# Kernel optimization log

Measured on AMD Instinct MI355X. Metric: run time of the kernel, lower is better.

The kernel has to match this reference:

```python
import jax, jax.numpy as jnp
import numpy as np

N = 50000          # nodes
E = 800000         # edges
H = 160            # hidden_dim = 32*5
HC = 32            # hidden_dim // 5 per-feature encoder width
LM = 768           # lm_input_dim
NUM_REL = 2
LEAK = 0.01        # nn.LeakyReLU default negative_slope


def leaky_relu(v):
    return jnp.where(v >= 0, v, LEAK * v)


def setup_inputs() -> dict:
    key = jax.random.key(0)
    ks = jax.random.split(key, 32)

    def lin(k, din, dout):
        kw, _ = jax.random.split(k)
        s = 1.0 / np.sqrt(din)
        W = jax.random.uniform(kw, (din, dout), jnp.float32, -s, s)
        b = jnp.zeros((dout,), jnp.float32)
        return W, b

    inp = {}
    inp["pre_x"] = jax.random.normal(ks[0], (N, LM), jnp.float32)
    inp["x"] = jnp.zeros((N, H), jnp.float32)  # dead input (overwritten in forward)
    inp["edge_index"] = jax.random.randint(ks[1], (2, E), 0, N, jnp.int32)
    inp["edge_type"] = jax.random.randint(ks[2], (E,), 0, NUM_REL, jnp.int32)
    inp["num_prop"] = jax.random.normal(ks[3], (N, 6), jnp.float32)
    inp["num_category"] = jax.random.normal(ks[4], (N, 11), jnp.float32)
    inp["des_tensor"] = jax.random.normal(ks[5], (N, LM), jnp.float32)
    inp["tweet_tensor"] = jax.random.normal(ks[6], (N, LM), jnp.float32)

    inp["W_np"], inp["b_np"] = lin(ks[7], 6, HC)
    inp["W_nc"], inp["b_nc"] = lin(ks[8], 11, HC)
    inp["W_des"], inp["b_des"] = lin(ks[9], LM, HC)
    inp["W_text"], inp["b_text"] = lin(ks[10], LM, HC)
    inp["W_tweet"], inp["b_tweet"] = lin(ks[11], LM, HC)
    inp["W_in"], inp["b_in"] = lin(ks[12], H, H)

    s = 1.0 / np.sqrt(H)
    inp["W_rel1"] = jax.random.uniform(ks[13], (NUM_REL, H, H), jnp.float32, -s, s)
    inp["W_root1"], inp["b_conv1"] = lin(ks[14], H, H)
    inp["W_rel2"] = jax.random.uniform(ks[15], (NUM_REL, H, H), jnp.float32, -s, s)
    inp["W_root2"], inp["b_conv2"] = lin(ks[16], H, H)

    inp["W_o1"], inp["b_o1"] = lin(ks[17], H, 80)
    inp["W_o2"], inp["b_o2"] = lin(ks[18], 80, 2)
    return inp


def rgcn_conv(h, src, dst, edge_type, W_rel, W_root, b):
    # PyG RGCNConv: per-relation mean aggregation + root transform + bias.
    out = h @ W_root + b
    for r in range(NUM_REL):
        w = (edge_type == r).astype(h.dtype)              # [E]
        msg = (h @ W_rel[r])[src] * w[:, None]            # [E, H] gather of transformed feats
        summed = jax.ops.segment_sum(msg, dst, num_segments=N)
        cnt = jax.ops.segment_sum(w, dst, num_segments=N)
        out = out + summed / jnp.maximum(cnt, 1.0)[:, None]
    return out


def reference(pre_x, x, edge_index, edge_type, num_prop, num_category, des_tensor,
              tweet_tensor, W_np, b_np, W_nc, b_nc, W_des, b_des, W_text, b_text,
              W_tweet, b_tweet, W_in, b_in, W_rel1, W_root1, b_conv1,
              W_rel2, W_root2, b_conv2, W_o1, b_o1, W_o2, b_o2):
    # Dropout is identity at inference.
    n = leaky_relu(num_prop @ W_np + b_np)
    c = leaky_relu(num_category @ W_nc + b_nc)
    d = leaky_relu(des_tensor @ W_des + b_des)
    tw = leaky_relu(tweet_tensor @ W_text + b_text)
    pre_t = leaky_relu(pre_x @ W_tweet + b_tweet)
    h = jnp.concatenate((n, c, d, tw, pre_t), axis=1)     # [N, 160]
    h = leaky_relu(h @ W_in + b_in)

    src, dst = edge_index[0], edge_index[1]
    h = rgcn_conv(h, src, dst, edge_type, W_rel1, W_root1, b_conv1)
    h = rgcn_conv(h, src, dst, edge_type, W_rel2, W_root2, b_conv2)

    em = leaky_relu(h @ W_o1 + b_o1)                      # [N, 80]
    out = em @ W_o2 + b_o2                                # [N, 2]
    return out, em
```

## Files before the change

### kernel.cpp

```cpp
#include <hip/hip_runtime.h>

#define NN 50000
#define EE 800000
#define HH 160
#define LMD 768
#define NBLK 196

typedef __attribute__((ext_vector_type(8))) short s8;
typedef __attribute__((ext_vector_type(4))) float f4;

__device__ __forceinline__ float lrelu(float v){ return v >= 0.f ? v : 0.01f*v; }

__device__ __forceinline__ short f2b(float f){
  unsigned int u = __float_as_uint(f);
  unsigned int r = (u + 0x7fffu + ((u >> 16) & 1u)) >> 16;
  return (short)r;
}
__device__ __forceinline__ float b2f(short s){
  return __uint_as_float(((unsigned int)(unsigned short)s) << 16);
}

struct WD { const float* s; short* d; int K; int C; };
struct WDs { WD w[11]; };
__global__ __launch_bounds__(256) void wt_k(WDs ds)
{
  WD w = ds.w[blockIdx.y];
  int idx = blockIdx.x*256 + threadIdx.x;
  if (idx < w.K * w.C) {
    int k = idx / w.C, c = idx - k*w.C;
    w.d[(size_t)c*w.K + k] = f2b(w.s[idx]);
  }
}

__global__ __launch_bounds__(256) void enc_small_k(
    const float* __restrict__ npx, const float* __restrict__ ncx,
    const float* __restrict__ Wnp, const float* __restrict__ bnp,
    const float* __restrict__ Wnc, const float* __restrict__ bnc,
    short* __restrict__ out)
{
  int gid = blockIdx.x*256 + threadIdx.x;
  int row = gid >> 6, c = gid & 63;
  if (row >= NN) return;
  float acc;
  if (c < 32) {
    acc = bnp[c];
    #pragma unroll
    for (int k = 0; k < 6; ++k) acc += npx[row*6+k]*Wnp[k*32+c];
  } else {
    int cc = c - 32;
    acc = bnc[cc];
    #pragma unroll
    for (int k = 0; k < 11; ++k) acc += ncx[row*11+k]*Wnc[k*32+cc];
  }
  out[(size_t)row*HH + c] = f2b(lrelu(acc));
}

template<int C, bool XBF, bool OUTF32>
__global__ __launch_bounds__(256) void mgemm_k(
    const void* __restrict__ Xv, int ldx,
    const short* __restrict__ WT, const float* __restrict__ bias,
    void* __restrict__ outv, int ldo, int K, int leaky)
{
  constexpr int NT = C/16;
  __shared__ __attribute__((aligned(16))) short Xs[128*40];
  __shared__ __attribute__((aligned(16))) short Ws[C*40];
  const int t = threadIdx.x;
  const int r0 = blockIdx.x*128;
  const int w = t >> 6, L = t & 63;
  const int lm = L & 15, lq = L >> 4;

  f4 acc[2][NT];
  #pragma unroll
  for (int i = 0; i < 2; ++i)
    #pragma unroll
    for (int j = 0; j < NT; ++j) acc[i][j] = (f4){0.f,0.f,0.f,0.f};

  for (int k0 = 0; k0 < K; k0 += 32) {
    #pragma unroll
    for (int i = t; i < 512; i += 256) {
      int row = i >> 2, kg = i & 3;
      int gr = r0 + row;
      s8 v;
      if (gr < NN) {
        if (XBF) {
          v = *(const s8*)((const short*)Xv + (size_t)gr*ldx + k0 + kg*8);
        } else {
          const float* xp = (const float*)Xv + (size_t)gr*ldx + k0 + kg*8;
          float4 a = *(const float4*)xp;
          float4 b = *(const float4*)(xp+4);
          v[0]=f2b(a.x); v[1]=f2b(a.y); v[2]=f2b(a.z); v[3]=f2b(a.w);
          v[4]=f2b(b.x); v[5]=f2b(b.y); v[6]=f2b(b.z); v[7]=f2b(b.w);
        }
      } else {
        v = (s8){0,0,0,0,0,0,0,0};
      }
      *(s8*)&Xs[row*40 + kg*8] = v;
    }
    for (int i = t; i < C*4; i += 256) {
      int c = i >> 2, kg = i & 3;
      *(s8*)&Ws[c*40 + kg*8] = *(const s8*)(WT + (size_t)c*K + k0 + kg*8);
    }
    __syncthreads();
    s8 a0 = *(const s8*)&Xs[(w*32 + lm)*40 + lq*8];
    s8 a1 = *(const s8*)&Xs[(w*32 + 16 + lm)*40 + lq*8];
    #pragma unroll
    for (int j = 0; j < NT; ++j) {
      s8 bf = *(const s8*)&Ws[(j*16 + lm)*40 + lq*8];
      acc[0][j] = __builtin_amdgcn_mfma_f32_16x16x32_bf16(a0, bf, acc[0][j], 0, 0, 0);
      acc[1][j] = __builtin_amdgcn_mfma_f32_16x16x32_bf16(a1, bf, acc[1][j], 0, 0, 0);
    }
    __syncthreads();
  }

  #pragma unroll
  for (int i = 0; i < 2; ++i) {
    #pragma unroll
    for (int j = 0; j < NT; ++j) {
      int col = j*16 + lm;
      float bv = bias ? bias[col] : 0.f;
      #pragma unroll
      for (int r = 0; r < 4; ++r) {
        int gr = r0 + w*32 + i*16 + lq*4 + r;
        if (gr < NN) {
          float v = acc[i][j][r] + bv;
          if (leaky) v = lrelu(v);
          if (OUTF32) ((float*)outv)[(size_t)gr*ldo + col] = v;
          else        ((short*)outv)[(size_t)gr*ldo + col] = f2b(v);
        }
      }
    }
  }
}

__global__ __launch_bounds__(256) void hist_k(
    const int* __restrict__ dst, const int* __restrict__ et, int* __restrict__ cnt2)
{
  int e = blockIdx.x*256 + threadIdx.x;
  if (e < EE) atomicAdd(&cnt2[et[e]*NN + dst[e]], 1);
}

__global__ __launch_bounds__(256) void inv_k(
    const int* __restrict__ cnt2, float* __restrict__ inv2, int* __restrict__ cntall)
{
  int i = blockIdx.x*256 + threadIdx.x;
  if (i >= NN) return;
  int c0 = cnt2[i], c1 = cnt2[NN + i];
  inv2[i]      = 1.f / (float)max(c0, 1);
  inv2[NN + i] = 1.f / (float)max(c1, 1);
  cntall[i] = c0 + c1;
}

__global__ __launch_bounds__(256) void scan1_k(
    const int* __restrict__ cntall, int* __restrict__ off1, int* __restrict__ partials)
{
  __shared__ int sh[256];
  int t = threadIdx.x;
  int i = blockIdx.x*256 + t;
  sh[t] = (i < NN) ? cntall[i] : 0;
  __syncthreads();
  for (int s = 1; s < 256; s <<= 1) {
    int add = (t >= s) ? sh[t-s] : 0;
    __syncthreads();
    sh[t] += add;
    __syncthreads();
  }
  if (i < NN) off1[i] = sh[t];
  if (t == 255) partials[blockIdx.x] = sh[255];
}

__global__ __launch_bounds__(256) void scan2_k(int* __restrict__ partials)
{
  __shared__ int sh[256];
  int t = threadIdx.x;
  sh[t] = (t < NBLK) ? partials[t] : 0;
  __syncthreads();
  for (int s = 1; s < 256; s <<= 1) {
    int add = (t >= s) ? sh[t-s] : 0;
    __syncthreads();
    sh[t] += add;
    __syncthreads();
  }
  if (t < NBLK) partials[t] = (t == 0) ? 0 : sh[t-1];
}

__global__ __launch_bounds__(256) void scan3_k(
    int* __restrict__ off, int* __restrict__ cursor, const int* __restrict__ partials)
{
  int i = blockIdx.x*256 + threadIdx.x;
  if (i < NN) {
    int v = off[i+1] + partials[i >> 8];
    off[i+1] = v;
    if (i + 1 < NN) cursor[i+1] = v;
  }
  if (i == 0) { off[0] = 0; cursor[0] = 0; }
}

__global__ __launch_bounds__(256) void scatter_k(
    const int* __restrict__ src, const int* __restrict__ dst, const int* __restrict__ et,
    int* __restrict__ cursor, int* __restrict__ elist)
{
  int e = blockIdx.x*256 + threadIdx.x;
  if (e >= EE) return;
  int d = dst[e];
  int pos = atomicAdd(&cursor[d], 1);
  elist[pos] = (src[e] << 1) | et[e];
}

__global__ __launch_bounds__(256) void aggregate_k(
    const int* __restrict__ off, const int* __restrict__ elist,
    const float* __restrict__ inv2,
    const short* __restrict__ t0, const short* __restrict__ t1,
    short* __restrict__ acc)
{
  int gid = blockIdx.x*256 + threadIdx.x;
  int d = gid / 20, q = gid - d*20;
  if (d >= NN) return;
  int beg = off[d], end = off[d+1];
  float i0 = inv2[d], i1 = inv2[NN + d];
  short* ap = acc + (size_t)d*HH + q*8;
  s8 rv = *(const s8*)ap;
  float a[8];
  #pragma unroll
  for (int i = 0; i < 8; ++i) a[i] = b2f(rv[i]);
  for (int p = beg; p < end; ++p) {
    int pk = elist[p];
    int s = pk >> 1;
    const short* tb = (pk & 1) ? t1 : t0;
    float sc = (pk & 1) ? i1 : i0;
    s8 v = *(const s8*)(tb + (size_t)s*HH + q*8);
    #pragma unroll
    for (int i = 0; i < 8; ++i) a[i] += b2f(v[i]) * sc;
  }
  s8 o;
  #pragma unroll
  for (int i = 0; i < 8; ++i) o[i] = f2b(a[i]);
  *(s8*)ap = o;
}

__global__ __launch_bounds__(256) void final_k(
    const float* __restrict__ em, const float* __restrict__ W,
    const float* __restrict__ b, float* __restrict__ out)
{
  int row = blockIdx.x*256 + threadIdx.x;
  if (row >= NN) return;
  float a0 = b[0], a1 = b[1];
  const float* e = em + (size_t)row*80;
  #pragma unroll
  for (int k = 0; k < 80; ++k) { float v = e[k]; a0 += v*W[k*2]; a1 += v*W[k*2+1]; }
  out[row*2] = a0; out[row*2+1] = a1;
}

extern "C" void kernel_launch(void* const* d_in, const int* in_sizes, int n_in,
                              void* d_out, int out_size, void* d_ws, size_t ws_size,
                              hipStream_t stream)
{
  const float* pre_x   = (const float*)d_in[0];
  const int*   eidx    = (const int*)d_in[2];
  const int*   etype   = (const int*)d_in[3];
  const float* num_prop= (const float*)d_in[4];
  const float* num_cat = (const float*)d_in[5];
  const float* des     = (const float*)d_in[6];
  const float* tweet   = (const float*)d_in[7];
  const float* W_np=(const float*)d_in[8],  *b_np=(const float*)d_in[9];
  const float* W_nc=(const float*)d_in[10], *b_nc=(const float*)d_in[11];
  const float* W_des=(const float*)d_in[12],*b_des=(const float*)d_in[13];
  const float* W_text=(const float*)d_in[14],*b_text=(const float*)d_in[15];
  const float* W_tweet=(const float*)d_in[16],*b_tweet=(const float*)d_in[17];
  const float* W_in=(const float*)d_in[18], *b_in=(const float*)d_in[19];
  const float* W_rel1=(const float*)d_in[20], *W_root1=(const float*)d_in[21], *b_c1=(const float*)d_in[22];
  const float* W_rel2=(const float*)d_in[23], *W_root2=(const float*)d_in[24], *b_c2=(const float*)d_in[25];
  const float* W_o1=(const float*)d_in[26], *b_o1=(const float*)d_in[27];
  const float* W_o2=(const float*)d_in[28], *b_o2=(const float*)d_in[29];

  float* out = (float*)d_out;
  float* em  = out + (size_t)NN*2;

  short* A  = (short*)d_ws;
  short* Bb = A  + (size_t)NN*HH;
  short* T0 = Bb + (size_t)NN*HH;
  short* T1 = T0 + (size_t)NN*HH;
  short* WT = T1 + (size_t)NN*HH;
  short* WT_des    = WT;
  short* WT_text   = WT +  24576;
  short* WT_tweet  = WT +  49152;
  short* WT_in     = WT +  73728;
  short* WT_root1  = WT +  99328;
  short* WT_rel1_0 = WT + 124928;
  short* WT_rel1_1 = WT + 150528;
  short* WT_root2  = WT + 176128;
  short* WT_rel2_0 = WT + 201728;
  short* WT_rel2_1 = WT + 227328;
  short* WT_o1     = WT + 252928;

  int*   cnt2    = (int*)(WT + 265728);
  float* inv2    = (float*)(cnt2 + 2*NN);
  int*   cntall  = (int*)(inv2 + 2*NN);
  int*   off     = cntall + NN;
  int*   partials= off + NN + 1;
  int*   cursor  = partials + 256;
  int*   elist   = cursor + NN;

  const int* src = eidx;
  const int* dst = eidx + EE;

  WDs ds;
  ds.w[0]  = (WD){W_des,          WT_des,    LMD, 32};
  ds.w[1]  = (WD){W_text,         WT_text,   LMD, 32};
  ds.w[2]  = (WD){W_tweet,        WT_tweet,  LMD, 32};
  ds.w[3]  = (WD){W_in,           WT_in,     HH, HH};
  ds.w[4]  = (WD){W_root1,        WT_root1,  HH, HH};
  ds.w[5]  = (WD){W_rel1,         WT_rel1_0, HH, HH};
  ds.w[6]  = (WD){W_rel1 + HH*HH, WT_rel1_1, HH, HH};
  ds.w[7]  = (WD){W_root2,        WT_root2,  HH, HH};
  ds.w[8]  = (WD){W_rel2,         WT_rel2_0, HH, HH};
  ds.w[9]  = (WD){W_rel2 + HH*HH, WT_rel2_1, HH, HH};
  ds.w[10] = (WD){W_o1,           WT_o1,     HH, 80};
  wt_k<<<dim3(100, 11), 256, 0, stream>>>(ds);

  hipMemsetAsync(cnt2, 0, 2*NN*sizeof(int), stream);
  hist_k  <<<(EE+255)/256, 256, 0, stream>>>(dst, etype, cnt2);
  inv_k   <<<NBLK, 256, 0, stream>>>(cnt2, inv2, cntall);
  scan1_k <<<NBLK, 256, 0, stream>>>(cntall, off+1, partials);
  scan2_k <<<1,    256, 0, stream>>>(partials);
  scan3_k <<<NBLK, 256, 0, stream>>>(off, cursor, partials);
  scatter_k<<<(EE+255)/256, 256, 0, stream>>>(src, dst, etype, cursor, elist);

  enc_small_k<<<(NN*64+255)/256, 256, 0, stream>>>(num_prop, num_cat, W_np,b_np, W_nc,b_nc, A);
  const int GB = (NN + 127) / 128;
  mgemm_k<32,false,false><<<GB,256,0,stream>>>(des,   LMD, WT_des,   b_des,   A+64,  HH, LMD, 1);
  mgemm_k<32,false,false><<<GB,256,0,stream>>>(tweet, LMD, WT_text,  b_text,  A+96,  HH, LMD, 1);
  mgemm_k<32,false,false><<<GB,256,0,stream>>>(pre_x, LMD, WT_tweet, b_tweet, A+128, HH, LMD, 1);

  mgemm_k<160,true,false><<<GB,256,0,stream>>>(A, HH, WT_in, b_in, Bb, HH, HH, 1);

  mgemm_k<160,true,false><<<GB,256,0,stream>>>(Bb, HH, WT_root1, b_c1, A, HH, HH, 0);
  mgemm_k<160,true,false><<<GB,256,0,stream>>>(Bb, HH, WT_rel1_0, nullptr, T0, HH, HH, 0);
  mgemm_k<160,true,false><<<GB,256,0,stream>>>(Bb, HH, WT_rel1_1, nullptr, T1, HH, HH, 0);
  aggregate_k<<<(NN*20+255)/256, 256, 0, stream>>>(off, elist, inv2, T0, T1, A);

  mgemm_k<160,true,false><<<GB,256,0,stream>>>(A, HH, WT_root2, b_c2, Bb, HH, HH, 0);
  mgemm_k<160,true,false><<<GB,256,0,stream>>>(A, HH, WT_rel2_0, nullptr, T0, HH, HH, 0);
  mgemm_k<160,true,false><<<GB,256,0,stream>>>(A, HH, WT_rel2_1, nullptr, T1, HH, HH, 0);
  aggregate_k<<<(NN*20+255)/256, 256, 0, stream>>>(off, elist, inv2, T0, T1, Bb);

  mgemm_k<80,true,true><<<GB,256,0,stream>>>(Bb, HH, WT_o1, b_o1, em, 80, HH, 1);
  final_k<<<NBLK, 256, 0, stream>>>(em, W_o2, b_o2, out);
}
```

Measured before the change: 949.7 us.

## Aggregate before transform and fuse root/relation GEMMs into one K=480 GEMM

Reorders each RGCN layer to first aggregate raw node features per relation (mean) into a concatenated [h | agg0 | agg1] buffer, then run one GEMM with a stacked [W_root; W_rel0; W_rel1] weight of K=480. This replaces three separate GEMMs plus a read-modify-write aggregation with one GEMM and a write-only aggregation, and it gathers from a single table. The output head GEMM and the final 80->2 projection are fused into one kernel using shared memory. The change adds a wider GEMM K and more workspace per node, and the aggregation now runs on pre-transform activations, which shifts where bf16 rounding happens.

```diff
diff --git a/kernel.cpp b/kernel.cpp
--- a/kernel.cpp
+++ b/kernel.cpp
@@ -20,7 +20,7 @@
   return __uint_as_float(((unsigned int)(unsigned short)s) << 16);
 }
 
-struct WD { const float* s; short* d; int K; int C; };
+struct WD { const float* s; short* d; int K; int C; int ldd; };
 struct WDs { WD w[11]; };
 __global__ __launch_bounds__(256) void wt_k(WDs ds)
 {
@@ -28,7 +28,7 @@
   int idx = blockIdx.x*256 + threadIdx.x;
   if (idx < w.K * w.C) {
     int k = idx / w.C, c = idx - k*w.C;
-    w.d[(size_t)c*w.K + k] = f2b(w.s[idx]);
+    w.d[(size_t)c*w.ldd + k] = f2b(w.s[idx]);
   }
 }
 
@@ -55,11 +55,11 @@
   out[(size_t)row*HH + c] = f2b(lrelu(acc));
 }
 
-template<int C, bool XBF, bool OUTF32>
+template<int C, bool XBF>
 __global__ __launch_bounds__(256) void mgemm_k(
     const void* __restrict__ Xv, int ldx,
     const short* __restrict__ WT, const float* __restrict__ bias,
-    void* __restrict__ outv, int ldo, int K, int leaky)
+    short* __restrict__ outb, int ldo, int K, int leaky)
 {
   constexpr int NT = C/16;
   __shared__ __attribute__((aligned(16))) short Xs[128*40];
@@ -76,7 +76,6 @@
     for (int j = 0; j < NT; ++j) acc[i][j] = (f4){0.f,0.f,0.f,0.f};
 
   for (int k0 = 0; k0 < K; k0 += 32) {
-    #pragma unroll
     for (int i = t; i < 512; i += 256) {
       int row = i >> 2, kg = i & 3;
       int gr = r0 + row;
@@ -124,10 +123,87 @@
         if (gr < NN) {
           float v = acc[i][j][r] + bv;
           if (leaky) v = lrelu(v);
-          if (OUTF32) ((float*)outv)[(size_t)gr*ldo + col] = v;
-          else        ((short*)outv)[(size_t)gr*ldo + col] = f2b(v);
+          outb[(size_t)gr*ldo + col] = f2b(v);
         }
       }
+    }
+  }
+}
+
+__global__ __launch_bounds__(256) void head_k(
+    const short* __restrict__ X,
+    const short* __restrict__ WT, const float* __restrict__ bias,
+    const float* __restrict__ W2, const float* __restrict__ b2,
+    float* __restrict__ em, float* __restrict__ out)
+{
+  constexpr int C = 80, NT = 5;
+  __shared__ __attribute__((aligned(16))) short Xs[128*40];
+  __shared__ __attribute__((aligned(16))) short Ws[C*40];
+  __shared__ float emS[128][81];
+  const int t = threadIdx.x;
+  const int r0 = blockIdx.x*128;
+  const int w = t >> 6, L = t & 63;
+  const int lm = L & 15, lq = L >> 4;
+
+  f4 acc[2][NT];
+  #pragma unroll
+  for (int i = 0; i < 2; ++i)
+    #pragma unroll
+    for (int j = 0; j < NT; ++j) acc[i][j] = (f4){0.f,0.f,0.f,0.f};
+
+  for (int k0 = 0; k0 < HH; k0 += 32) {
+    for (int i = t; i < 512; i += 256) {
+      int row = i >> 2, kg = i & 3;
+      int gr = r0 + row;
+      s8 v = (s8){0,0,0,0,0,0,0,0};
+      if (gr < NN) v = *(const s8*)(X + (size_t)gr*HH + k0 + kg*8);
+      *(s8*)&Xs[row*40 + kg*8] = v;
+    }
+    for (int i = t; i < C*4; i += 256) {
+      int c = i >> 2, kg = i & 3;
+      *(s8*)&Ws[c*40 + kg*8] = *(const s8*)(WT + (size_t)c*HH + k0 + kg*8);
+    }
+    __syncthreads();
+    s8 a0 = *(const s8*)&Xs[(w*32 + lm)*40 + lq*8];
+    s8 a1 = *(const s8*)&Xs[(w*32 + 16 + lm)*40 + lq*8];
+    #pragma unroll
+    for (int j = 0; j < NT; ++j) {
+      s8 bf = *(const s8*)&Ws[(j*16 + lm)*40 + lq*8];
+      acc[0][j] = __builtin_amdgcn_mfma_f32_16x16x32_bf16(a0, bf, acc[0][j], 0, 0, 0);
+      acc[1][j] = __builtin_amdgcn_mfma_f32_16x16x32_bf16(a1, bf, acc[1][j], 0, 0, 0);
+    }
+    __syncthreads();
+  }
+
+  #pragma unroll
+  for (int i = 0; i < 2; ++i) {
+    #pragma unroll
+    for (int j = 0; j < NT; ++j) {
+      int col = j*16 + lm;
+      float bv = bias[col];
+      #pragma unroll
+      for (int r = 0; r < 4; ++r) {
+        int lr = w*32 + i*16 + lq*4 + r;
+        int gr = r0 + lr;
+        if (gr < NN) {
+          float v = lrelu(acc[i][j][r] + bv);
+          em[(size_t)gr*80 + col] = v;
+          emS[lr][col] = v;
+        }
+      }
+    }
+  }
+  __syncthreads();
+  if (t < 128) {
+    int gr = r0 + t;
+    if (gr < NN) {
+      float a0 = b2[0], a1 = b2[1];
+      #pragma unroll
+      for (int k = 0; k < 80; ++k) {
+        float v = emS[t][k];
+        a0 += v*W2[k*2]; a1 += v*W2[k*2+1];
+      }
+      out[gr*2] = a0; out[gr*2+1] = a1;
     }
   }
 }
@@ -208,46 +284,32 @@
 
 __global__ __launch_bounds__(256) void aggregate_k(
     const int* __restrict__ off, const int* __restrict__ elist,
-    const float* __restrict__ inv2,
-    const short* __restrict__ t0, const short* __restrict__ t1,
-    short* __restrict__ acc)
+    const float* __restrict__ inv2, short* __restrict__ X)
 {
   int gid = blockIdx.x*256 + threadIdx.x;
   int d = gid / 20, q = gid - d*20;
   if (d >= NN) return;
   int beg = off[d], end = off[d+1];
-  float i0 = inv2[d], i1 = inv2[NN + d];
-  short* ap = acc + (size_t)d*HH + q*8;
-  s8 rv = *(const s8*)ap;
-  float a[8];
-  #pragma unroll
-  for (int i = 0; i < 8; ++i) a[i] = b2f(rv[i]);
+  float a0[8], a1[8];
+  #pragma unroll
+  for (int i = 0; i < 8; ++i) { a0[i] = 0.f; a1[i] = 0.f; }
   for (int p = beg; p < end; ++p) {
     int pk = elist[p];
     int s = pk >> 1;
-    const short* tb = (pk & 1) ? t1 : t0;
-    float sc = (pk & 1) ? i1 : i0;
-    s8 v = *(const s8*)(tb + (size_t)s*HH + q*8);
-    #pragma unroll
-    for (int i = 0; i < 8; ++i) a[i] += b2f(v[i]) * sc;
-  }
-  s8 o;
-  #pragma unroll
-  for (int i = 0; i < 8; ++i) o[i] = f2b(a[i]);
-  *(s8*)ap = o;
-}
-
-__global__ __launch_bounds__(256) void final_k(
-    const float* __restrict__ em, const float* __restrict__ W,
-    const float* __restrict__ b, float* __restrict__ out)
-{
-  int row = blockIdx.x*256 + threadIdx.x;
-  if (row >= NN) return;
-  float a0 = b[0], a1 = b[1];
-  const float* e = em + (size_t)row*80;
-  #pragma unroll
-  for (int k = 0; k < 80; ++k) { float v = e[k]; a0 += v*W[k*2]; a1 += v*W[k*2+1]; }
-  out[row*2] = a0; out[row*2+1] = a1;
+    float m1 = (float)(pk & 1), m0 = 1.f - m1;
+    s8 v = *(const s8*)(X + (size_t)s*480 + q*8);
+    #pragma unroll
+    for (int i = 0; i < 8; ++i) {
+      float f = b2f(v[i]);
+      a0[i] += f*m0; a1[i] += f*m1;
+    }
+  }
+  float i0 = inv2[d], i1 = inv2[NN + d];
+  s8 o0, o1;
+  #pragma unroll
+  for (int i = 0; i < 8; ++i) { o0[i] = f2b(a0[i]*i0); o1[i] = f2b(a1[i]*i1); }
+  *(s8*)(X + (size_t)d*480 + 160 + q*8) = o0;
+  *(s8*)(X + (size_t)d*480 + 320 + q*8) = o1;
 }
 
 extern "C" void kernel_launch(void* const* d_in, const int* in_sizes, int n_in,
@@ -275,22 +337,17 @@
   float* out = (float*)d_out;
   float* em  = out + (size_t)NN*2;
 
-  short* A  = (short*)d_ws;
-  short* Bb = A  + (size_t)NN*HH;
-  short* T0 = Bb + (size_t)NN*HH;
-  short* T1 = T0 + (size_t)NN*HH;
-  short* WT = T1 + (size_t)NN*HH;
-  short* WT_des    = WT;
-  short* WT_text   = WT +  24576;
-  short* WT_tweet  = WT +  49152;
-  short* WT_in     = WT +  73728;
-  short* WT_root1  = WT +  99328;
-  short* WT_rel1_0 = WT + 124928;
-  short* WT_rel1_1 = WT + 150528;
-  short* WT_root2  = WT + 176128;
-  short* WT_rel2_0 = WT + 201728;
-  short* WT_rel2_1 = WT + 227328;
-  short* WT_o1     = WT + 252928;
+  short* Acat = (short*)d_ws;
+  short* X1   = Acat + (size_t)NN*HH;
+  short* X2   = X1   + (size_t)NN*480;
+  short* WT   = X2   + (size_t)NN*480;
+  short* WT_des   = WT;
+  short* WT_text  = WT +  24576;
+  short* WT_tweet = WT +  49152;
+  short* WT_in    = WT +  73728;
+  short* WT_cat1  = WT +  99328;
+  short* WT_cat2  = WT + 176128;
+  short* WT_o1    = WT + 252928;
 
   int*   cnt2    = (int*)(WT + 265728);
   float* inv2    = (float*)(cnt2 + 2*NN);
@@ -304,17 +361,17 @@
   const int* dst = eidx + EE;
 
   WDs ds;
-  ds.w[0]  = (WD){W_des,          WT_des,    LMD, 32};
-  ds.w[1]  = (WD){W_text,         WT_text,   LMD, 32};
-  ds.w[2]  = (WD){W_tweet,        WT_tweet,  LMD, 32};
-  ds.w[3]  = (WD){W_in,           WT_in,     HH, HH};
-  ds.w[4]  = (WD){W_root1,        WT_root1,  HH, HH};
-  ds.w[5]  = (WD){W_rel1,         WT_rel1_0, HH, HH};
-  ds.w[6]  = (WD){W_rel1 + HH*HH, WT_rel1_1, HH, HH};
-  ds.w[7]  = (WD){W_root2,        WT_root2,  HH, HH};
-  ds.w[8]  = (WD){W_rel2,         WT_rel2_0, HH, HH};
-  ds.w[9]  = (WD){W_rel2 + HH*HH, WT_rel2_1, HH, HH};
-  ds.w[10] = (WD){W_o1,           WT_o1,     HH, 80};
+  ds.w[0]  = (WD){W_des,          WT_des,         LMD, 32, LMD};
+  ds.w[1]  = (WD){W_text,         WT_text,        LMD, 32, LMD};
+  ds.w[2]  = (WD){W_tweet,        WT_tweet,       LMD, 32, LMD};
+  ds.w[3]  = (WD){W_in,           WT_in,          HH, HH, HH};
+  ds.w[4]  = (WD){W_root1,        WT_cat1,        HH, HH, 480};
+  ds.w[5]  = (WD){W_rel1,         WT_cat1 + 160,  HH, HH, 480};
+  ds.w[6]  = (WD){W_rel1 + HH*HH, WT_cat1 + 320,  HH, HH, 480};
+  ds.w[7]  = (WD){W_root2,        WT_cat2,        HH, HH, 480};
+  ds.w[8]  = (WD){W_rel2,         WT_cat2 + 160,  HH, HH, 480};
+  ds.w[9]  = (WD){W_rel2 + HH*HH, WT_cat2 + 320,  HH, HH, 480};
+  ds.w[10] = (WD){W_o1,           WT_o1,          HH, 80, HH};
   wt_k<<<dim3(100, 11), 256, 0, stream>>>(ds);
 
   hipMemsetAsync(cnt2, 0, 2*NN*sizeof(int), stream);
@@ -325,24 +382,19 @@
   scan3_k <<<NBLK, 256, 0, stream>>>(off, cursor, partials);
   scatter_k<<<(EE+255)/256, 256, 0, stream>>>(src, dst, etype, cursor, elist);
 
-  enc_small_k<<<(NN*64+255)/256, 256, 0, stream>>>(num_prop, num_cat, W_np,b_np, W_nc,b_nc, A);
+  enc_small_k<<<(NN*64+255)/256, 256, 0, stream>>>(num_prop, num_cat, W_np,b_np, W_nc,b_nc, Acat);
   const int GB = (NN + 127) / 128;
-  mgemm_k<32,false,false><<<GB,256,0,stream>>>(des,   LMD, WT_des,   b_des,   A+64,  HH, LMD, 1);
-  mgemm_k<32,false,false><<<GB,256,0,stream>>>(tweet, LMD, WT_text,  b_text,  A+96,  HH, LMD, 1);
-  mgemm_k<32,false,false><<<GB,256,0,stream>>>(pre_x, LMD, WT_tweet, b_tweet, A+128, HH, LMD, 1);
-
-  mgemm_k<160,true,false><<<GB,256,0,stream>>>(A, HH, WT_in, b_in, Bb, HH, HH, 1);
-
-  mgemm_k<160,true,false><<<GB,256,0,stream>>>(Bb, HH, WT_root1, b_c1, A, HH, HH, 0);
-  mgemm_k<160,true,false><<<GB,256,0,stream>>>(Bb, HH, WT_rel1_0, nullptr, T0, HH, HH, 0);
-  mgemm_k<160,true,false><<<GB,256,0,stream>>>(Bb, HH, WT_rel1_1, nullptr, T1, HH, HH, 0);
-  aggregate_k<<<(NN*20+255)/256, 256, 0, stream>>>(off, elist, inv2, T0, T1, A);
-
-  mgemm_k<160,true,false><<<GB,256,0,stream>>>(A, HH, WT_root2, b_c2, Bb, HH, HH, 0);
-  mgemm_k<160,true,false><<<GB,256,0,stream>>>(A, HH, WT_rel2_0, nullptr, T0, HH, HH, 0);
-  mgemm_k<160,true,false><<<GB,256,0,stream>>>(A, HH, WT_rel2_1, nullptr, T1, HH, HH, 0);
-  aggregate_k<<<(NN*20+255)/256, 256, 0, stream>>>(off, elist, inv2, T0, T1, Bb);
-
-  mgemm_k<80,true,true><<<GB,256,0,stream>>>(Bb, HH, WT_o1, b_o1, em, 80, HH, 1);
-  final_k<<<NBLK, 256, 0, stream>>>(em, W_o2, b_o2, out);
-}
+  mgemm_k<32,false><<<GB,256,0,stream>>>(des,   LMD, WT_des,   b_des,   Acat+64,  HH, LMD, 1);
+  mgemm_k<32,false><<<GB,256,0,stream>>>(tweet, LMD, WT_text,  b_text,  Acat+96,  HH, LMD, 1);
+  mgemm_k<32,false><<<GB,256,0,stream>>>(pre_x, LMD, WT_tweet, b_tweet, Acat+128, HH, LMD, 1);
+
+  mgemm_k<160,true><<<GB,256,0,stream>>>(Acat, HH, WT_in, b_in, X1, 480, HH, 1);
+
+  aggregate_k<<<(NN*20+255)/256, 256, 0, stream>>>(off, elist, inv2, X1);
+  mgemm_k<160,true><<<GB,256,0,stream>>>(X1, 480, WT_cat1, b_c1, X2, 480, 480, 0);
+
+  aggregate_k<<<(NN*20+255)/256, 256, 0, stream>>>(off, elist, inv2, X2);
+  mgemm_k<160,true><<<GB,256,0,stream>>>(X2, 480, WT_cat2, b_c2, Acat, HH, 480, 0);
+
+  head_k<<<GB,256,0,stream>>>(Acat, WT_o1, b_o1, W_o2, b_o2, em, out);
+}
```

Measured after the change: 908.9 us. 4.3% less time.
